# Kernel optimization log

Measured on AMD Instinct MI355X. Metric: run time of the kernel, lower is better.

Reference implementation:

```python
import jax, jax.numpy as jnp
import numpy as np

N_DIFFS = 8388608
N_BINS = 1000
EPS = 1e-4


def setup_inputs() -> dict:
    key = jax.random.key(0)
    k1, k2 = jax.random.split(key)
    # bin centers are probabilities strictly inside (0,1) so logit is finite
    bin_centers = 0.01 + 0.98 * jax.random.uniform(k1, (N_BINS,), dtype=jnp.float32)
    obs_idx = jax.random.randint(k2, (N_DIFFS, 3), 0, N_BINS, dtype=jnp.int64)
    # per-operator params, init as in the torch module: lb=-10, ub=+10 for bounds 1..3
    lower_bounds = -10.0 * jnp.ones((3,), dtype=jnp.float32)
    upper_bounds = 10.0 * jnp.ones((3,), dtype=jnp.float32)
    return {
        "bin_centers": bin_centers,
        "observation_probability_index": obs_idx,
        "lower_bounds": lower_bounds,
        "upper_bounds": upper_bounds,
    }


def reference(bin_centers, observation_probability_index, lower_bounds, upper_bounds):
    # get_parameters swaps (lb, ub) in place if lb > ub -> effective min/max
    lb = jnp.minimum(lower_bounds, upper_bounds)  # [3]
    ub = jnp.maximum(lower_bounds, upper_bounds)  # [3]
    # logit of the gathered task requirements: [n_diffs, 3]
    t = bin_centers[observation_probability_index]
    g = jnp.log(t / (1.0 - t))
    # sigmoid((ub - logit(t)) / (ub - lb + eps)) per bound, product over the 3 bounds
    x = (ub - g) / (ub - lb + EPS)
    return jnp.prod(jax.nn.sigmoid(x), axis=1)  # [n_diffs]
```

## Files before the change

### kernel.cpp

```cpp
#include <hip/hip_runtime.h>


#define EPS 1e-4f

__global__ __launch_bounds__(256) void pm_kernel(
    const float* __restrict__ bc,
    const int*   __restrict__ idx,
    const float* __restrict__ lo,
    const float* __restrict__ hi,
    float*       __restrict__ out,
    int nbins, int ndiffs)
{
    __shared__ float tab[3][1024];

    const float lb0 = fminf(lo[0], hi[0]), ub0 = fmaxf(lo[0], hi[0]);
    const float lb1 = fminf(lo[1], hi[1]), ub1 = fmaxf(lo[1], hi[1]);
    const float lb2 = fminf(lo[2], hi[2]), ub2 = fmaxf(lo[2], hi[2]);
    const float r0 = 1.0f / (ub0 - lb0 + EPS);
    const float r1 = 1.0f / (ub1 - lb1 + EPS);
    const float r2 = 1.0f / (ub2 - lb2 + EPS);

    for (int b = threadIdx.x; b < nbins; b += blockDim.x) {
        const float t = bc[b];
        const float g = __logf(t / (1.0f - t));
        tab[0][b] = 1.0f / (1.0f + __expf(-(ub0 - g) * r0));
        tab[1][b] = 1.0f / (1.0f + __expf(-(ub1 - g) * r1));
        tab[2][b] = 1.0f / (1.0f + __expf(-(ub2 - g) * r2));
    }
    __syncthreads();

    const int tid    = blockIdx.x * blockDim.x + threadIdx.x;
    const int stride = gridDim.x * blockDim.x;
    const int nvec   = ndiffs >> 2;

    const int4* __restrict__ idx4 = (const int4*)idx;
    float4*     __restrict__ out4 = (float4*)out;

    for (int v = tid; v < nvec; v += stride) {
        const int4 a = idx4[3 * v + 0];
        const int4 b = idx4[3 * v + 1];
        const int4 c = idx4[3 * v + 2];
        float4 r;
        r.x = tab[0][a.x] * tab[1][a.y] * tab[2][a.z];
        r.y = tab[0][a.w] * tab[1][b.x] * tab[2][b.y];
        r.z = tab[0][b.z] * tab[1][b.w] * tab[2][c.x];
        r.w = tab[0][c.y] * tab[1][c.z] * tab[2][c.w];
        out4[v] = r;
    }

    for (int i = (nvec << 2) + tid; i < ndiffs; i += stride) {
        const int i0 = idx[3 * i + 0];
        const int i1 = idx[3 * i + 1];
        const int i2 = idx[3 * i + 2];
        out[i] = tab[0][i0] * tab[1][i1] * tab[2][i2];
    }
}

extern "C" void kernel_launch(void* const* d_in, const int* in_sizes, int n_in,
                              void* d_out, int out_size, void* d_ws, size_t ws_size,
                              hipStream_t stream)
{
    const float* bc  = (const float*)d_in[0];
    const int*   idx = (const int*)  d_in[1];
    const float* lo  = (const float*)d_in[2];
    const float* hi  = (const float*)d_in[3];
    float*       out = (float*)d_out;

    const int nbins  = in_sizes[0];
    const int ndiffs = out_size;

    const int nvec   = ndiffs >> 2;
    int blocks = (nvec + 255) / 256;
    if (blocks < 1) blocks = 1;

    pm_kernel<<<blocks, 256, 0, stream>>>(bc, idx, lo, hi, out, nbins, ndiffs);
}
```

Before: 162.4 us.

## Stage index loads through shared memory for coalescing and use persistent grid

Each wavefront now loads its 64x12 index block with fully coalesced int4 loads into a per-wave shared-memory staging buffer, then each lane reads its own 12 indices back from LDS. Before, each lane loaded three strided int4s. The launch also switches from one block per 1024 outputs to a fixed grid of 2048 blocks with a grid-stride loop, so the per-block table build runs fewer times. In exchange it adds LDS traffic, with possible bank conflicts from the stride-12 reads, and uses more shared memory per block, which may lower occupancy.

```diff
diff --git a/kernel.cpp b/kernel.cpp
--- a/kernel.cpp
+++ b/kernel.cpp
@@ -2,8 +2,11 @@
 
 
 #define EPS 1e-4f
+#define TPB 256
+#define NBLK 2048
+#define BINCAP 1024
 
-__global__ __launch_bounds__(256) void pm_kernel(
+__global__ __launch_bounds__(TPB) void pm_kernel(
     const float* __restrict__ bc,
     const int*   __restrict__ idx,
     const float* __restrict__ lo,
@@ -11,7 +14,8 @@
     float*       __restrict__ out,
     int nbins, int ndiffs)
 {
-    __shared__ float tab[3][1024];
+    __shared__ float tab[3][BINCAP];
+    __shared__ int   stage[TPB * 12];
 
     const float lb0 = fminf(lo[0], hi[0]), ub0 = fmaxf(lo[0], hi[0]);
     const float lb1 = fminf(lo[1], hi[1]), ub1 = fmaxf(lo[1], hi[1]);
@@ -20,39 +24,55 @@
     const float r1 = 1.0f / (ub1 - lb1 + EPS);
     const float r2 = 1.0f / (ub2 - lb2 + EPS);
 
-    for (int b = threadIdx.x; b < nbins; b += blockDim.x) {
+    for (int b = threadIdx.x; b < nbins; b += TPB) {
         const float t = bc[b];
         const float g = __logf(t / (1.0f - t));
-        tab[0][b] = 1.0f / (1.0f + __expf(-(ub0 - g) * r0));
-        tab[1][b] = 1.0f / (1.0f + __expf(-(ub1 - g) * r1));
-        tab[2][b] = 1.0f / (1.0f + __expf(-(ub2 - g) * r2));
+        tab[0][b] = 1.0f / (1.0f + __expf((g - ub0) * r0));
+        tab[1][b] = 1.0f / (1.0f + __expf((g - ub1) * r1));
+        tab[2][b] = 1.0f / (1.0f + __expf((g - ub2) * r2));
     }
     __syncthreads();
 
-    const int tid    = blockIdx.x * blockDim.x + threadIdx.x;
-    const int stride = gridDim.x * blockDim.x;
+    const int tid    = blockIdx.x * TPB + threadIdx.x;
+    const int stride = gridDim.x * TPB;
+    const int lane   = threadIdx.x & 63;
     const int nvec   = ndiffs >> 2;
 
     const int4* __restrict__ idx4 = (const int4*)idx;
     float4*     __restrict__ out4 = (float4*)out;
 
-    for (int v = tid; v < nvec; v += stride) {
-        const int4 a = idx4[3 * v + 0];
-        const int4 b = idx4[3 * v + 1];
-        const int4 c = idx4[3 * v + 2];
-        float4 r;
-        r.x = tab[0][a.x] * tab[1][a.y] * tab[2][a.z];
-        r.y = tab[0][a.w] * tab[1][b.x] * tab[2][b.y];
-        r.z = tab[0][b.z] * tab[1][b.w] * tab[2][c.x];
-        r.w = tab[0][c.y] * tab[1][c.z] * tab[2][c.w];
-        out4[v] = r;
+    int4*      s4 = (int4*)(stage + (threadIdx.x >> 6) * (64 * 12));
+    const int* my = (const int*)s4 + 12 * lane;
+
+    for (int v = tid; v - lane < nvec; v += stride) {
+        const int wbase = v - lane;
+        if (wbase + 64 <= nvec) {
+            const int b3 = 3 * wbase;
+            const int4 q0 = idx4[b3 + lane];
+            const int4 q1 = idx4[b3 + 64 + lane];
+            const int4 q2 = idx4[b3 + 128 + lane];
+            s4[lane]       = q0;
+            s4[lane + 64]  = q1;
+            s4[lane + 128] = q2;
+            float4 r;
+            r.x = tab[0][my[0]] * tab[1][my[1]]  * tab[2][my[2]];
+            r.y = tab[0][my[3]] * tab[1][my[4]]  * tab[2][my[5]];
+            r.z = tab[0][my[6]] * tab[1][my[7]]  * tab[2][my[8]];
+            r.w = tab[0][my[9]] * tab[1][my[10]] * tab[2][my[11]];
+            out4[v] = r;
+        } else if (v < nvec) {
+            const int4 a = idx4[3*v], b = idx4[3*v+1], c = idx4[3*v+2];
+            float4 r;
+            r.x = tab[0][a.x] * tab[1][a.y] * tab[2][a.z];
+            r.y = tab[0][a.w] * tab[1][b.x] * tab[2][b.y];
+            r.z = tab[0][b.z] * tab[1][b.w] * tab[2][c.x];
+            r.w = tab[0][c.y] * tab[1][c.z] * tab[2][c.w];
+            out4[v] = r;
+        }
     }
 
     for (int i = (nvec << 2) + tid; i < ndiffs; i += stride) {
-        const int i0 = idx[3 * i + 0];
-        const int i1 = idx[3 * i + 1];
-        const int i2 = idx[3 * i + 2];
-        out[i] = tab[0][i0] * tab[1][i1] * tab[2][i2];
+        out[i] = tab[0][idx[3*i]] * tab[1][idx[3*i+1]] * tab[2][idx[3*i+2]];
     }
 }
 
@@ -69,9 +89,5 @@
     const int nbins  = in_sizes[0];
     const int ndiffs = out_size;
 
-    const int nvec   = ndiffs >> 2;
-    int blocks = (nvec + 255) / 256;
-    if (blocks < 1) blocks = 1;
-
-    pm_kernel<<<blocks, 256, 0, stream>>>(bc, idx, lo, hi, out, nbins, ndiffs);
+    pm_kernel<<<NBLK, TPB, 0, stream>>>(bc, idx, lo, hi, out, nbins, ndiffs);
 }
```

After: 165.8 us. 2.1% more time.

## Use fixed persistent grid with one element per thread and int3 loads

Applied to the files above, without the earlier changes.

Replaces the one-block-per-1024-elements launch with a fixed grid of 2048 blocks that grid-strides over the data, so each block's shared table build is amortized over many elements instead of being redone by 8192 blocks. The inner loop now handles one output per iteration with an int3 index load and a scalar store, instead of three int4 loads and a float4 store. This cuts redundant table setup (log/exp per bin per block) but gives up the wider vector loads and stores, which may reduce memory efficiency.

```diff
diff --git a/kernel.cpp b/kernel.cpp
--- a/kernel.cpp
+++ b/kernel.cpp
@@ -2,8 +2,11 @@
 
 
 #define EPS 1e-4f
+#define TPB 256
+#define NBLK 2048
+#define BINCAP 1024
 
-__global__ __launch_bounds__(256) void pm_kernel(
+__global__ __launch_bounds__(TPB) void pm_kernel(
     const float* __restrict__ bc,
     const int*   __restrict__ idx,
     const float* __restrict__ lo,
@@ -11,7 +14,9 @@
     float*       __restrict__ out,
     int nbins, int ndiffs)
 {
-    __shared__ float tab[3][1024];
+    __shared__ float tab0[BINCAP];
+    __shared__ float tab1[BINCAP];
+    __shared__ float tab2[BINCAP];
 
     const float lb0 = fminf(lo[0], hi[0]), ub0 = fmaxf(lo[0], hi[0]);
     const float lb1 = fminf(lo[1], hi[1]), ub1 = fmaxf(lo[1], hi[1]);
@@ -20,39 +25,23 @@
     const float r1 = 1.0f / (ub1 - lb1 + EPS);
     const float r2 = 1.0f / (ub2 - lb2 + EPS);
 
-    for (int b = threadIdx.x; b < nbins; b += blockDim.x) {
+    for (int b = threadIdx.x; b < nbins; b += TPB) {
         const float t = bc[b];
         const float g = __logf(t / (1.0f - t));
-        tab[0][b] = 1.0f / (1.0f + __expf(-(ub0 - g) * r0));
-        tab[1][b] = 1.0f / (1.0f + __expf(-(ub1 - g) * r1));
-        tab[2][b] = 1.0f / (1.0f + __expf(-(ub2 - g) * r2));
+        tab0[b] = 1.0f / (1.0f + __expf((g - ub0) * r0));
+        tab1[b] = 1.0f / (1.0f + __expf((g - ub1) * r1));
+        tab2[b] = 1.0f / (1.0f + __expf((g - ub2) * r2));
     }
     __syncthreads();
 
-    const int tid    = blockIdx.x * blockDim.x + threadIdx.x;
-    const int stride = gridDim.x * blockDim.x;
-    const int nvec   = ndiffs >> 2;
+    const int tid    = blockIdx.x * TPB + threadIdx.x;
+    const int stride = NBLK * TPB;
 
-    const int4* __restrict__ idx4 = (const int4*)idx;
-    float4*     __restrict__ out4 = (float4*)out;
+    const int3* __restrict__ idx3 = (const int3*)idx;
 
-    for (int v = tid; v < nvec; v += stride) {
-        const int4 a = idx4[3 * v + 0];
-        const int4 b = idx4[3 * v + 1];
-        const int4 c = idx4[3 * v + 2];
-        float4 r;
-        r.x = tab[0][a.x] * tab[1][a.y] * tab[2][a.z];
-        r.y = tab[0][a.w] * tab[1][b.x] * tab[2][b.y];
-        r.z = tab[0][b.z] * tab[1][b.w] * tab[2][c.x];
-        r.w = tab[0][c.y] * tab[1][c.z] * tab[2][c.w];
-        out4[v] = r;
-    }
-
-    for (int i = (nvec << 2) + tid; i < ndiffs; i += stride) {
-        const int i0 = idx[3 * i + 0];
-        const int i1 = idx[3 * i + 1];
-        const int i2 = idx[3 * i + 2];
-        out[i] = tab[0][i0] * tab[1][i1] * tab[2][i2];
+    for (int i = tid; i < ndiffs; i += stride) {
+        const int3 v = idx3[i];
+        out[i] = tab0[v.x] * tab1[v.y] * tab2[v.z];
     }
 }
 
@@ -66,12 +55,5 @@
     const float* hi  = (const float*)d_in[3];
     float*       out = (float*)d_out;
 
-    const int nbins  = in_sizes[0];
-    const int ndiffs = out_size;
-
-    const int nvec   = ndiffs >> 2;
-    int blocks = (nvec + 255) / 256;
-    if (blocks < 1) blocks = 1;
-
-    pm_kernel<<<blocks, 256, 0, stream>>>(bc, idx, lo, hi, out, nbins, ndiffs);
+    pm_kernel<<<NBLK, TPB, 0, stream>>>(bc, idx, lo, hi, out, in_sizes[0], out_size);
 }
```

Result: slower. 166.3 us (+2.4%).
